# Kernel optimization log

Hardware: AMD Instinct MI355X
Metric: run time of the kernel (lower is better)

The kernel has to match this reference:

```python
import jax, jax.numpy as jnp
import numpy as np

T, B, D, N = 2048, 16, 1024, 64
EPS = 1e-6


def setup_inputs() -> dict:
    key = jax.random.key(0)
    k1, k2 = jax.random.split(key)
    x = jax.random.normal(k1, (T, B, D), dtype=jnp.float32)
    S0 = jnp.zeros((B, N, N), dtype=jnp.float32)
    # xavier-uniform-ish scale for each [N, D] block of the fused projection
    limit = float(np.sqrt(6.0 / (N + D)))
    W_kvqg = jax.random.uniform(k2, (4 * N, D), dtype=jnp.float32, minval=-limit, maxval=limit)
    b_gate = jnp.full((N,), 2.0, dtype=jnp.float32)
    return {"x": x, "S0": S0, "W_kvqg": W_kvqg, "b_gate": b_gate}


def _silu(z):
    return z * jax.nn.sigmoid(z)


def reference(x, S0, W_kvqg, b_gate):
    n = b_gate.shape[0]
    # fused projection: [T, B, 4n]
    proj = jnp.einsum('tbd,nd->tbn', x, W_kvqg)
    k_all = proj[..., :n]
    v_all = proj[..., n:2 * n]
    q_all = proj[..., 2 * n:3 * n]
    g_all = proj[..., 3 * n:]

    def step(S, inp):
        k, v, q, g = inp
        decay = jax.nn.sigmoid(g + b_gate)                      # [B, n]
        k_norm = k / (jnp.linalg.norm(k, axis=-1, keepdims=True) + EPS)
        retrieved = jnp.einsum('bij,bj->bi', S, k_norm)         # [B, n]
        delta = v - retrieved
        S = decay[:, :, None] * S + delta[:, :, None] * k_norm[:, None, :]
        Sq = jnp.einsum('bij,bj->bi', S, q)                     # [B, n]
        out = Sq * _silu(Sq)
        return S, out

    S_final, output = jax.lax.scan(step, S0, (k_all, v_all, q_all, g_all))
    return output, S_final
```

## Files before the change

### kernel.cpp

```cpp
#include <hip/hip_runtime.h>
#include <hip/hip_bf16.h>
#include <math.h>

#define T_STEPS 2048
#define B_SZ 16
#define D_SZ 1024
#define N_SZ 64
#define M_ROWS (T_STEPS * B_SZ)
#define NOUT (4 * N_SZ)
#define U_BLK 8
#define NBLK (T_STEPS / U_BLK)
#define TSTR 17

typedef __attribute__((ext_vector_type(8))) short bf16x8;
typedef __attribute__((ext_vector_type(4))) float f32x4;

template <int CTRL, int RMASK, bool BC>
__device__ __forceinline__ float dpp_add(float v) {
  return v + __int_as_float(__builtin_amdgcn_update_dpp(
                 0, __float_as_int(v), CTRL, RMASK, 0xF, BC));
}
__device__ __forceinline__ float wave_red(float v) {
  v = dpp_add<0xB1, 0xF, true>(v);
  v = dpp_add<0x4E, 0xF, true>(v);
  v = dpp_add<0x141, 0xF, true>(v);
  v = dpp_add<0x140, 0xF, true>(v);
  v = dpp_add<0x142, 0xA, false>(v);
  v = dpp_add<0x143, 0xC, false>(v);
  return __int_as_float(__builtin_amdgcn_readlane(__float_as_int(v), 63));
}

__device__ __forceinline__ unsigned cvt2(float a, float b) {
  float2 f; f.x = a; f.y = b;
  __hip_bfloat162 h = __float22bfloat162_rn(f);
  return *reinterpret_cast<unsigned*>(&h);
}

__global__ __launch_bounds__(256) void wcvt(const float* __restrict__ W,
                                            unsigned* __restrict__ Wb) {
  const size_t idx = ((size_t)blockIdx.x * 256 + threadIdx.x) * 4;
  const float4 f = *reinterpret_cast<const float4*>(&W[idx]);
  uint2 o;
  o.x = cvt2(f.x, f.y);
  o.y = cvt2(f.z, f.w);
  *reinterpret_cast<uint2*>(&Wb[idx >> 1]) = o;
}

__global__ __launch_bounds__(256) void gemm_proj(const float* __restrict__ x,
                                                 const unsigned short* __restrict__ Wb,
                                                 float* __restrict__ proj) {
  __shared__ unsigned short Al[64][72];
  __shared__ unsigned short Bl[256][72];
  const int tid = threadIdx.x;
  const int lane = tid & 63;
  const int wv = tid >> 6;
  const int m0 = blockIdx.x * 64;
  const int nw0 = wv * 64;

  f32x4 acc[4][4];
#pragma unroll
  for (int m = 0; m < 4; ++m)
#pragma unroll
    for (int n = 0; n < 4; ++n) acc[m][n] = (f32x4){0.f, 0.f, 0.f, 0.f};

  const int arow = tid >> 2;
  const int akb = (tid & 3) * 16;

  for (int k0 = 0; k0 < D_SZ; k0 += 64) {
    {
      const float* src = &x[(size_t)(m0 + arow) * D_SZ + k0 + akb];
      unsigned tmp[8];
#pragma unroll
      for (int c = 0; c < 4; ++c) {
        const float4 f = *reinterpret_cast<const float4*>(src + c * 4);
        tmp[2 * c] = cvt2(f.x, f.y);
        tmp[2 * c + 1] = cvt2(f.z, f.w);
      }
      *reinterpret_cast<float4*>(&Al[arow][akb]) =
          *reinterpret_cast<const float4*>(&tmp[0]);
      *reinterpret_cast<float4*>(&Al[arow][akb + 8]) =
          *reinterpret_cast<const float4*>(&tmp[4]);
    }
    {
      const unsigned short* src = &Wb[(size_t)tid * D_SZ + k0];
#pragma unroll
      for (int h = 0; h < 8; ++h)
        *reinterpret_cast<float4*>(&Bl[tid][h * 8]) =
            *reinterpret_cast<const float4*>(&src[h * 8]);
    }
    __syncthreads();
    const int fr = lane & 15;
#pragma unroll
    for (int kk = 0; kk < 64; kk += 32) {
      const int kof = kk + (lane >> 4) * 8;
      bf16x8 af[4], bfr[4];
#pragma unroll
      for (int m = 0; m < 4; ++m)
        af[m] = *reinterpret_cast<const bf16x8*>(&Al[m * 16 + fr][kof]);
#pragma unroll
      for (int n = 0; n < 4; ++n)
        bfr[n] = *reinterpret_cast<const bf16x8*>(&Bl[nw0 + n * 16 + fr][kof]);
#pragma unroll
      for (int m = 0; m < 4; ++m)
#pragma unroll
        for (int n = 0; n < 4; ++n)
          acc[m][n] = __builtin_amdgcn_mfma_f32_16x16x32_bf16(
              af[m], bfr[n], acc[m][n], 0, 0, 0);
    }
    __syncthreads();
  }

  const int col = lane & 15;
  const int rb = (lane >> 4) * 4;
#pragma unroll
  for (int m = 0; m < 4; ++m)
#pragma unroll
    for (int n = 0; n < 4; ++n)
#pragma unroll
      for (int r = 0; r < 4; ++r)
        proj[(size_t)(m0 + m * 16 + rb + r) * NOUT + nw0 + n * 16 + col] =
            acc[m][n][r];
}

__global__ __launch_bounds__(512) void norm_gram(float* __restrict__ proj,
                                                 const float* __restrict__ b_gate,
                                                 float* __restrict__ gram) {
  const int u = threadIdx.x >> 6;
  const int lane = threadIdx.x & 63;
  const int grp = blockIdx.x;
  const int blk = grp & (NBLK - 1);
  const int b = grp >> 8;
  const int t0 = blk * U_BLK;
  const int m = (t0 + u) * B_SZ + b;

  __shared__ float lds_kn[U_BLK][64];

  float* p = proj + (size_t)m * NOUT;
  const float kf = p[lane];
  const float vf = p[64 + lane];
  const float qf = p[128 + lane];
  const float gf = p[192 + lane];
  const float bg = b_gate[lane];
  const float ss = wave_red(kf * kf);
  const float kn = kf / (sqrtf(ss) + 1e-6f);
  const float dec = 1.f / (1.f + expf(-(gf + bg)));
  asm volatile("s_waitcnt vmcnt(0)" ::: "memory");
  float2* pp = reinterpret_cast<float2*>(p);
  float2 a; a.x = kn; a.y = qf;
  float2 c; c.x = vf; c.y = dec;
  pp[lane] = a;
  pp[64 + lane] = c;

  lds_kn[u][lane] = kn;
  __syncthreads();

  float row[8];
#pragma unroll
  for (int cc = 0; cc < 8; ++cc) {
    const float knc = lds_kn[cc][lane];
    const float lhs = (cc > u) ? kn : qf;
    row[cc] = wave_red(lhs * knc);
  }
  if (lane == 0) {
    float* dst = gram + ((size_t)grp * 64 + u * 8);
    float4 r0, r1;
    r0.x = row[0]; r0.y = row[1]; r0.z = row[2]; r0.w = row[3];
    r1.x = row[4]; r1.y = row[5]; r1.z = row[6]; r1.w = row[7];
    *reinterpret_cast<float4*>(dst) = r0;
    *reinterpret_cast<float4*>(dst + 4) = r1;
  }
}

__global__ __launch_bounds__(256, 1) void scan_kernel(
    const float* __restrict__ proj, const float* __restrict__ gram,
    const float* __restrict__ S0, float* __restrict__ out,
    float* __restrict__ Sfin) {
  const int wid = threadIdx.x >> 6;
  const int lane = threadIdx.x & 63;
  const int bid = blockIdx.x;
  const int b = (bid & 7) | ((bid >> 7) << 3);
  const int i = (((bid >> 3) & 15) << 2) | wid;

  __shared__ float ldsT[2][64 * TSTR];
  __shared__ float ldsV[2][U_BLK * 128];
  __shared__ float ldsG[2][64];
  __shared__ float ldsS[4][64];

  float S = S0[(size_t)b * 4096 + i * 64 + lane];

  const int r0 = wid * 2;
  float4 st0, st1;
  float stg = 0.f;

#define STAGE_LOAD(blkv)                                                      \
  {                                                                           \
    const size_t g0 = ((size_t)(((blkv) * U_BLK + r0) * B_SZ + b)) * NOUT;    \
    st0 = *reinterpret_cast<const float4*>(&proj[g0 + lane * 4]);             \
    st1 = *reinterpret_cast<const float4*>(&proj[g0 + (size_t)B_SZ * NOUT +   \
                                                 lane * 4]);                  \
    if (wid == 0) stg = gram[((size_t)b * NBLK + (blkv)) * 64 + lane];        \
  }

#define STAGE_WRITE(bufv)                                                     \
  {                                                                           \
    if (lane < 32) {                                                          \
      const int j0 = lane * 2;                                                \
      ldsT[bufv][j0 * TSTR + r0] = st0.x;                                     \
      ldsT[bufv][j0 * TSTR + 8 + r0] = st0.y;                                 \
      ldsT[bufv][(j0 + 1) * TSTR + r0] = st0.z;                               \
      ldsT[bufv][(j0 + 1) * TSTR + 8 + r0] = st0.w;                           \
      ldsT[bufv][j0 * TSTR + r0 + 1] = st1.x;                                 \
      ldsT[bufv][j0 * TSTR + 8 + r0 + 1] = st1.y;                             \
      ldsT[bufv][(j0 + 1) * TSTR + r0 + 1] = st1.z;                           \
      ldsT[bufv][(j0 + 1) * TSTR + 8 + r0 + 1] = st1.w;                       \
    } else {                                                                  \
      *reinterpret_cast<float4*>(                                             \
          &ldsV[bufv][r0 * 128 + (lane - 32) * 4]) = st0;                     \
      *reinterpret_cast<float4*>(                                             \
          &ldsV[bufv][(r0 + 1) * 128 + (lane - 32) * 4]) = st1;               \
    }                                                                         \
    if (wid == 0) ldsG[bufv][lane] = stg;                                     \
  }

#define GM(idx) __int_as_float(                                               \
    __builtin_amdgcn_readlane(__float_as_int(gv), (idx)))

  STAGE_LOAD(0)
  STAGE_WRITE(0)
  __syncthreads();

  const int koff = (lane >> 4) * 8;
  const int col = lane & 15;

  for (int blk = 0; blk < NBLK; ++blk) {
    const int buf = blk & 1;
    if (blk + 1 < NBLK) STAGE_LOAD(blk + 1)

    ldsS[wid][lane] = S;
    asm volatile("s_waitcnt lgkmcnt(0)" ::: "memory");

    float2 vdv[8];
#pragma unroll
    for (int u = 0; u < 8; ++u)
      vdv[u] = *reinterpret_cast<const float2*>(&ldsV[buf][u * 128 + i * 2]);
    const float gv = ldsG[buf][lane];
    float knl[8];
#pragma unroll
    for (int w = 0; w < 8; ++w) knl[w] = ldsT[buf][lane * TSTR + w];

    f32x4 red = (f32x4){0.f, 0.f, 0.f, 0.f};
#pragma unroll
    for (int kk = 0; kk < 2; ++kk) {
      float a[8], bsrc[8];
      *reinterpret_cast<float4*>(&a[0]) = *reinterpret_cast<const float4*>(
          &ldsS[wid][kk * 32 + koff]);
      *reinterpret_cast<float4*>(&a[4]) = *reinterpret_cast<const float4*>(
          &ldsS[wid][kk * 32 + koff + 4]);
#pragma unroll
      for (int t = 0; t < 8; ++t)
        bsrc[t] = ldsT[buf][(kk * 32 + koff + t) * TSTR + col];
      union { unsigned u[4]; bf16x8 v; } cvA, cvB;
#pragma unroll
      for (int h = 0; h < 4; ++h) {
        asm("v_cvt_pk_bf16_f32 %0, %1, %2"
            : "=v"(cvA.u[h]) : "v"(a[2 * h]), "v"(a[2 * h + 1]));
        asm("v_cvt_pk_bf16_f32 %0, %1, %2"
            : "=v"(cvB.u[h]) : "v"(bsrc[2 * h]), "v"(bsrc[2 * h + 1]));
      }
      red = __builtin_amdgcn_mfma_f32_16x16x32_bf16(cvA.v, cvB.v, red, 0, 0, 0);
    }

    float c[9], rc[8];
    c[0] = 1.f;
#pragma unroll
    for (int u = 0; u < 8; ++u) {
      c[u + 1] = c[u] * vdv[u].y;
      rc[u] = __builtin_amdgcn_rcpf(c[u + 1]);
    }

    float acc[8], sac[8];
    const int ri = __float_as_int(red[0]);
#pragma unroll
    for (int u = 0; u < 8; ++u) {
      acc[u] = __int_as_float(__builtin_amdgcn_readlane(ri, u));
      sac[u] = __int_as_float(__builtin_amdgcn_readlane(ri, 8 + u));
    }

    float dp[8], sqv[8];
#pragma unroll
    for (int w = 0; w < 8; ++w) {
      const float d = fmaf(-c[w], acc[w], vdv[w].x);
      dp[w] = d * rc[w];
      sqv[w] = fmaf(c[w + 1], sac[w], d * GM(w * 8 + w));
#pragma unroll
      for (int u = w + 1; u < 8; ++u) {
        acc[u] = fmaf(dp[w], GM(w * 8 + u), acc[u]);
        sac[u] = fmaf(dp[w], GM(u * 8 + w), sac[u]);
      }
    }
    float tacc = S;
#pragma unroll
    for (int w = 0; w < 8; ++w) tacc = fmaf(dp[w], knl[w], tacc);
    S = c[8] * tacc;

    if (lane == 0) {
      const size_t ob = (size_t)blk * U_BLK * (B_SZ * N_SZ) + b * N_SZ + i;
#pragma unroll
      for (int u = 0; u < 8; ++u)
        out[ob + (size_t)u * (B_SZ * N_SZ)] = sqv[u];
    }

    if (blk + 1 < NBLK) STAGE_WRITE(buf ^ 1)
    __syncthreads();
  }

  Sfin[(size_t)b * 4096 + i * 64 + lane] = S;
#undef STAGE_LOAD
#undef STAGE_WRITE
#undef GM
}

__global__ __launch_bounds__(256) void silu_pp(float* __restrict__ o) {
  const size_t idx = ((size_t)blockIdx.x * 256 + threadIdx.x) * 4;
  float4 v = *reinterpret_cast<float4*>(&o[idx]);
  v.x = v.x * v.x * __fdividef(1.f, 1.f + __expf(-v.x));
  v.y = v.y * v.y * __fdividef(1.f, 1.f + __expf(-v.y));
  v.z = v.z * v.z * __fdividef(1.f, 1.f + __expf(-v.z));
  v.w = v.w * v.w * __fdividef(1.f, 1.f + __expf(-v.w));
  *reinterpret_cast<float4*>(&o[idx]) = v;
}

extern "C" void kernel_launch(void* const* d_in, const int* in_sizes, int n_in,
                              void* d_out, int out_size, void* d_ws, size_t ws_size,
                              hipStream_t stream) {
  const float* x      = (const float*)d_in[0];
  const float* S0     = (const float*)d_in[1];
  const float* W      = (const float*)d_in[2];
  const float* b_gate = (const float*)d_in[3];
  float* out  = (float*)d_out;
  float* proj = (float*)d_ws;
  float* gram = (float*)((char*)d_ws + (size_t)M_ROWS * NOUT * 4);
  unsigned* Wb = (unsigned*)((char*)d_ws + 35u * 1024 * 1024);

  hipLaunchKernelGGL(wcvt, dim3(256), dim3(256), 0, stream, W, Wb);
  hipLaunchKernelGGL(gemm_proj, dim3(M_ROWS / 64), dim3(256), 0, stream,
                     x, (const unsigned short*)Wb, proj);
  hipLaunchKernelGGL(norm_gram, dim3(B_SZ * NBLK), dim3(512), 0, stream,
                     proj, b_gate, gram);
  hipLaunchKernelGGL(scan_kernel, dim3(256), dim3(256), 0, stream,
                     proj, gram, S0, out, out + (size_t)T_STEPS * B_SZ * N_SZ);
  hipLaunchKernelGGL(silu_pp, dim3(2048), dim3(256), 0, stream, out);
}
```

Measured before the change: 341.4 us.

## Fuse key normalization and gate sigmoid into GEMM epilogue, fold SiLU into scan

Moves the k-normalization and decay sigmoid into the projection GEMM epilogue. Each wave owns one of the k/v/q/g column blocks, and results are exchanged through reused shared memory so the GEMM writes the interleaved (kn,q),(v,dec) layout directly. The separate norm_gram kernel becomes a gram-only kernel with one wave per row. The SiLU post-pass is folded into the scan's output store, which is spread over 8 lanes. This removes a read-modify-write pass over proj and a full pass over the output, at the cost of a heavier GEMM epilogue with idle waves and an extra block barrier.

```diff
diff --git a/kernel.cpp b/kernel.cpp
--- a/kernel.cpp
+++ b/kernel.cpp
@@ -29,6 +29,13 @@
   v = dpp_add<0x143, 0xC, false>(v);
   return __int_as_float(__builtin_amdgcn_readlane(__float_as_int(v), 63));
 }
+__device__ __forceinline__ float red16(float v) {
+  v = dpp_add<0xB1, 0xF, true>(v);
+  v = dpp_add<0x4E, 0xF, true>(v);
+  v = dpp_add<0x141, 0xF, true>(v);
+  v = dpp_add<0x140, 0xF, true>(v);
+  return v;
+}
 
 __device__ __forceinline__ unsigned cvt2(float a, float b) {
   float2 f; f.x = a; f.y = b;
@@ -46,11 +53,15 @@
   *reinterpret_cast<uint2*>(&Wb[idx >> 1]) = o;
 }
 
-__global__ __launch_bounds__(256) void gemm_proj(const float* __restrict__ x,
-                                                 const unsigned short* __restrict__ Wb,
-                                                 float* __restrict__ proj) {
-  __shared__ unsigned short Al[64][72];
-  __shared__ unsigned short Bl[256][72];
+__global__ __launch_bounds__(256) void gemm_proj(
+    const float* __restrict__ x, const unsigned short* __restrict__ Wb,
+    float* __restrict__ proj, const float* __restrict__ b_gate) {
+  __shared__ char smem[46080];
+  auto Al = (unsigned short (*)[72])smem;
+  auto Bl = (unsigned short (*)[72])(smem + 9216);
+  auto knb = (float (*)[68])smem;
+  auto decb = (float (*)[68])(smem + 17408);
+
   const int tid = threadIdx.x;
   const int lane = tid & 63;
   const int wv = tid >> 6;
@@ -110,59 +121,96 @@
     __syncthreads();
   }
 
-  const int col = lane & 15;
-  const int rb = (lane >> 4) * 4;
-#pragma unroll
-  for (int m = 0; m < 4; ++m)
-#pragma unroll
-    for (int n = 0; n < 4; ++n)
-#pragma unroll
-      for (int r = 0; r < 4; ++r)
-        proj[(size_t)(m0 + m * 16 + rb + r) * NOUT + nw0 + n * 16 + col] =
-            acc[m][n][r];
-}
-
-__global__ __launch_bounds__(512) void norm_gram(float* __restrict__ proj,
-                                                 const float* __restrict__ b_gate,
-                                                 float* __restrict__ gram) {
-  const int u = threadIdx.x >> 6;
+  const int l15 = lane & 15;
+  const int lg = lane >> 4;
+  if (wv == 0) {
+#pragma unroll
+    for (int m = 0; m < 4; ++m)
+#pragma unroll
+      for (int r = 0; r < 4; ++r) {
+        float part = 0.f;
+#pragma unroll
+        for (int n = 0; n < 4; ++n)
+          part = fmaf(acc[m][n][r], acc[m][n][r], part);
+        const float ss = red16(part);
+        const float rk = 1.f / (sqrtf(ss) + 1e-6f);
+        const int row = m * 16 + lg * 4 + r;
+#pragma unroll
+        for (int n = 0; n < 4; ++n)
+          knb[row][n * 16 + l15] = acc[m][n][r] * rk;
+      }
+  } else if (wv == 3) {
+#pragma unroll
+    for (int m = 0; m < 4; ++m)
+#pragma unroll
+      for (int r = 0; r < 4; ++r) {
+        const int row = m * 16 + lg * 4 + r;
+#pragma unroll
+        for (int n = 0; n < 4; ++n) {
+          const float g = acc[m][n][r];
+          decb[row][n * 16 + l15] =
+              1.f / (1.f + expf(-(g + b_gate[n * 16 + l15])));
+        }
+      }
+  }
+  __syncthreads();
+  if (wv == 2) {
+#pragma unroll
+    for (int m = 0; m < 4; ++m)
+#pragma unroll
+      for (int r = 0; r < 4; ++r) {
+        const int row = m * 16 + lg * 4 + r;
+#pragma unroll
+        for (int n = 0; n < 4; ++n) {
+          const int qc = n * 16 + l15;
+          float2 pr; pr.x = knb[row][qc]; pr.y = acc[m][n][r];
+          *reinterpret_cast<float2*>(
+              &proj[(size_t)(m0 + row) * NOUT + qc * 2]) = pr;
+        }
+      }
+  } else if (wv == 1) {
+#pragma unroll
+    for (int m = 0; m < 4; ++m)
+#pragma unroll
+      for (int r = 0; r < 4; ++r) {
+        const int row = m * 16 + lg * 4 + r;
+#pragma unroll
+        for (int n = 0; n < 4; ++n) {
+          const int vc = n * 16 + l15;
+          float2 pr; pr.x = acc[m][n][r]; pr.y = decb[row][vc];
+          *reinterpret_cast<float2*>(
+              &proj[(size_t)(m0 + row) * NOUT + 128 + vc * 2]) = pr;
+        }
+      }
+  }
+}
+
+__global__ __launch_bounds__(256) void gram_kernel(const float* __restrict__ proj,
+                                                   float* __restrict__ gram) {
+  const int wid = threadIdx.x >> 6;
   const int lane = threadIdx.x & 63;
-  const int grp = blockIdx.x;
+  const int gw = blockIdx.x * 4 + wid;
+  const int a = gw & 7;
+  const int grp = gw >> 3;
   const int blk = grp & (NBLK - 1);
   const int b = grp >> 8;
   const int t0 = blk * U_BLK;
-  const int m = (t0 + u) * B_SZ + b;
-
-  __shared__ float lds_kn[U_BLK][64];
-
-  float* p = proj + (size_t)m * NOUT;
-  const float kf = p[lane];
-  const float vf = p[64 + lane];
-  const float qf = p[128 + lane];
-  const float gf = p[192 + lane];
-  const float bg = b_gate[lane];
-  const float ss = wave_red(kf * kf);
-  const float kn = kf / (sqrtf(ss) + 1e-6f);
-  const float dec = 1.f / (1.f + expf(-(gf + bg)));
-  asm volatile("s_waitcnt vmcnt(0)" ::: "memory");
-  float2* pp = reinterpret_cast<float2*>(p);
-  float2 a; a.x = kn; a.y = qf;
-  float2 c; c.x = vf; c.y = dec;
-  pp[lane] = a;
-  pp[64 + lane] = c;
-
-  lds_kn[u][lane] = kn;
-  __syncthreads();
+  const float2* base = reinterpret_cast<const float2*>(proj);
+
+  float2 knq[8];
+#pragma unroll
+  for (int c = 0; c < 8; ++c)
+    knq[c] = base[(size_t)((t0 + c) * B_SZ + b) * 128 + lane];
+  const float2 mine = knq[a];
 
   float row[8];
 #pragma unroll
-  for (int cc = 0; cc < 8; ++cc) {
-    const float knc = lds_kn[cc][lane];
-    const float lhs = (cc > u) ? kn : qf;
-    row[cc] = wave_red(lhs * knc);
+  for (int c = 0; c < 8; ++c) {
+    const float lhs = (c > a) ? mine.x : mine.y;
+    row[c] = wave_red(lhs * knq[c].x);
   }
   if (lane == 0) {
-    float* dst = gram + ((size_t)grp * 64 + u * 8);
+    float* dst = gram + ((size_t)grp * 64 + a * 8);
     float4 r0, r1;
     r0.x = row[0]; r0.y = row[1]; r0.z = row[2]; r0.w = row[3];
     r1.x = row[4]; r1.y = row[5]; r1.z = row[6]; r1.w = row[7];
@@ -303,11 +351,17 @@
     for (int w = 0; w < 8; ++w) tacc = fmaf(dp[w], knl[w], tacc);
     S = c[8] * tacc;
 
-    if (lane == 0) {
+    if (lane < 8) {
+      const float a0 = (lane & 1) ? sqv[1] : sqv[0];
+      const float a1 = (lane & 1) ? sqv[3] : sqv[2];
+      const float a2 = (lane & 1) ? sqv[5] : sqv[4];
+      const float a3 = (lane & 1) ? sqv[7] : sqv[6];
+      const float b0 = (lane & 2) ? a1 : a0;
+      const float b1 = (lane & 2) ? a3 : a2;
+      const float sq = (lane & 4) ? b1 : b0;
       const size_t ob = (size_t)blk * U_BLK * (B_SZ * N_SZ) + b * N_SZ + i;
-#pragma unroll
-      for (int u = 0; u < 8; ++u)
-        out[ob + (size_t)u * (B_SZ * N_SZ)] = sqv[u];
+      out[ob + (size_t)lane * (B_SZ * N_SZ)] =
+          sq * sq * __fdividef(1.f, 1.f + __expf(-sq));
     }
 
     if (blk + 1 < NBLK) STAGE_WRITE(buf ^ 1)
@@ -318,16 +372,6 @@
 #undef STAGE_LOAD
 #undef STAGE_WRITE
 #undef GM
-}
-
-__global__ __launch_bounds__(256) void silu_pp(float* __restrict__ o) {
-  const size_t idx = ((size_t)blockIdx.x * 256 + threadIdx.x) * 4;
-  float4 v = *reinterpret_cast<float4*>(&o[idx]);
-  v.x = v.x * v.x * __fdividef(1.f, 1.f + __expf(-v.x));
-  v.y = v.y * v.y * __fdividef(1.f, 1.f + __expf(-v.y));
-  v.z = v.z * v.z * __fdividef(1.f, 1.f + __expf(-v.z));
-  v.w = v.w * v.w * __fdividef(1.f, 1.f + __expf(-v.w));
-  *reinterpret_cast<float4*>(&o[idx]) = v;
 }
 
 extern "C" void kernel_launch(void* const* d_in, const int* in_sizes, int n_in,
@@ -344,10 +388,9 @@
 
   hipLaunchKernelGGL(wcvt, dim3(256), dim3(256), 0, stream, W, Wb);
   hipLaunchKernelGGL(gemm_proj, dim3(M_ROWS / 64), dim3(256), 0, stream,
-                     x, (const unsigned short*)Wb, proj);
-  hipLaunchKernelGGL(norm_gram, dim3(B_SZ * NBLK), dim3(512), 0, stream,
-                     proj, b_gate, gram);
+                     x, (const unsigned short*)Wb, proj, b_gate);
+  hipLaunchKernelGGL(gram_kernel, dim3(32768 / 4), dim3(256), 0, stream,
+                     proj, gram);
   hipLaunchKernelGGL(scan_kernel, dim3(256), dim3(256), 0, stream,
                      proj, gram, S0, out, out + (size_t)T_STEPS * B_SZ * N_SZ);
-  hipLaunchKernelGGL(silu_pp, dim3(2048), dim3(256), 0, stream, out);
-}
+}
```

New measurement: 358.4 us. 1.05x slower.
